# Kernel optimization log

Measured on AMD Instinct MI355X. Metric: run time of the kernel, lower is better.

## Reference

```python
import jax, jax.numpy as jnp
import numpy as np

N = 100_000   # nodes
E = 1_600_000 # edges
F = 128       # num_node_features
H = 128       # hidden_channels
C = 10        # num_classes
G = 128       # graphs in batch


def setup_inputs() -> dict:
    key = jax.random.key(0)
    ks = jax.random.split(key, 12)
    x = jax.random.normal(ks[0], (N, F), jnp.float32)
    edge_index = jax.random.randint(ks[1], (2, E), 0, N, dtype=jnp.int32)
    batch = jnp.sort(jax.random.randint(ks[2], (N,), 0, G, dtype=jnp.int32))
    s = 1.0 / np.sqrt(H)
    W0 = jax.random.normal(ks[3], (F, H), jnp.float32) * s
    b0 = jnp.zeros((H,), jnp.float32)
    W1 = jax.random.normal(ks[4], (H, H), jnp.float32) * s
    b1 = jnp.zeros((H,), jnp.float32)
    W2 = jax.random.normal(ks[5], (H, H), jnp.float32) * s
    b2 = jnp.zeros((H,), jnp.float32)
    Wlin = jax.random.normal(ks[6], (H, C), jnp.float32) * s
    blin = jnp.zeros((C,), jnp.float32)
    return {"x": x, "edge_index": edge_index, "batch": batch,
            "W0": W0, "b0": b0, "W1": W1, "b1": b1, "W2": W2, "b2": b2,
            "Wlin": Wlin, "blin": blin}


def gcn_conv(x, W, b, src, dst):
    """PyG GCNConv: symmetric-normalized aggregation with self-loops."""
    xw = x @ W  # [N, H]
    # degree from destination column, +1 for self-loop (gcn_norm)
    deg = jax.ops.segment_sum(jnp.ones(src.shape[0], xw.dtype), dst,
                              num_segments=N) + 1.0
    dinv = jax.lax.rsqrt(deg)  # deg^{-1/2}
    # edge messages: xw[src] * deg_src^{-1/2} * deg_dst^{-1/2}
    msg = xw[src] * (dinv[src] * dinv[dst])[:, None]  # [E, H]
    agg = jax.ops.segment_sum(msg, dst, num_segments=N)
    # self-loop contribution: xw * deg^{-1}
    return agg + xw * (dinv * dinv)[:, None] + b


def reference(x, edge_index, batch, W0, b0, W1, b1, W2, b2, Wlin, blin):
    src, dst = edge_index[0], edge_index[1]
    h = jax.nn.relu(gcn_conv(x, W0, b0, src, dst))
    h = jax.nn.relu(gcn_conv(h, W1, b1, src, dst))
    h = jax.nn.relu(gcn_conv(h, W2, b2, src, dst))
    # global_mean_pool over graph ids
    cnt = jax.ops.segment_sum(jnp.ones(N, h.dtype), batch, num_segments=G)
    pooled = jax.ops.segment_sum(h, batch, num_segments=G) / jnp.maximum(cnt, 1.0)[:, None]
    # dropout is identity in eval mode
    return pooled @ Wlin + blin  # [G, C]
```

## Files before the change

kernel.cpp:

```cpp
#include <hip/hip_runtime.h>

typedef short short8 __attribute__((ext_vector_type(8)));
typedef float f32x4 __attribute__((ext_vector_type(4)));

#define HDIM 128
#define SCAN_NB 256
#define SCAN_TPB 256

__device__ __forceinline__ ushort f2bf(float f) {
  uint u = __float_as_uint(f);
  u += 0x7fffu + ((u >> 16) & 1u);
  return (ushort)(u >> 16);
}
__device__ __forceinline__ float bflo(uint v){ return __uint_as_float(v << 16); }
__device__ __forceinline__ float bfhi(uint v){ return __uint_as_float(v & 0xffff0000u); }

__global__ __launch_bounds__(256) void k_deg(const int* __restrict__ dst, int E, int* __restrict__ degc) {
  for (int e = blockIdx.x*blockDim.x + threadIdx.x; e < E; e += gridDim.x*blockDim.x)
    atomicAdd(&degc[dst[e]], 1);
}

__global__ __launch_bounds__(256) void k_dinv(const int* __restrict__ degc, float* __restrict__ dinv, int N) {
  int i = blockIdx.x*256 + threadIdx.x;
  if (i < N) dinv[i] = rsqrtf((float)degc[i] + 1.0f);
}

__global__ __launch_bounds__(SCAN_TPB) void k_scanA(const int* __restrict__ degc, int N,
                                                    int* __restrict__ blocksum) {
  int ipt = (N + SCAN_NB*SCAN_TPB - 1) / (SCAN_NB*SCAN_TPB);
  int chunk = ipt * SCAN_TPB;
  int start = blockIdx.x * chunk + threadIdx.x * ipt;
  int s = 0;
  #pragma unroll
  for (int k = 0; k < 4; ++k) {
    if (k < ipt) { int i = start + k; if (i < N) s += degc[i]; }
  }
  __shared__ int red[SCAN_TPB];
  int t = threadIdx.x;
  red[t] = s; __syncthreads();
  for (int off = SCAN_TPB/2; off > 0; off >>= 1) {
    if (t < off) red[t] += red[t+off];
    __syncthreads();
  }
  if (t == 0) blocksum[blockIdx.x] = red[0];
}

__global__ __launch_bounds__(SCAN_NB) void k_scanB(const int* __restrict__ blocksum,
                                                   int* __restrict__ blockoff, int* __restrict__ totalN) {
  __shared__ int sh[SCAN_NB];
  int t = threadIdx.x;
  sh[t] = blocksum[t];
  __syncthreads();
  for (int off = 1; off < SCAN_NB; off <<= 1) {
    int v = (t >= off) ? sh[t-off] : 0;
    __syncthreads();
    sh[t] += v;
    __syncthreads();
  }
  blockoff[t] = (t == 0) ? 0 : sh[t-1];
  if (t == SCAN_NB-1) *totalN = sh[t];
}

__global__ __launch_bounds__(SCAN_TPB) void k_scanC(const int* __restrict__ degc, int N,
    const int* __restrict__ blockoff, const int* __restrict__ totalN, int* __restrict__ row_ptr) {
  int ipt = (N + SCAN_NB*SCAN_TPB - 1) / (SCAN_NB*SCAN_TPB);
  int chunk = ipt * SCAN_TPB;
  int start = blockIdx.x * chunk + threadIdx.x * ipt;
  int t = threadIdx.x;
  int vals[4];
  int s = 0;
  #pragma unroll
  for (int k = 0; k < 4; ++k) {
    int v = 0;
    if (k < ipt) { int i = start + k; if (i < N) v = degc[i]; }
    vals[k] = v; s += v;
  }
  __shared__ int sh[SCAN_TPB];
  sh[t] = s; __syncthreads();
  for (int off = 1; off < SCAN_TPB; off <<= 1) {
    int v = (t >= off) ? sh[t-off] : 0;
    __syncthreads();
    sh[t] += v;
    __syncthreads();
  }
  int run = blockoff[blockIdx.x] + ((t == 0) ? 0 : sh[t-1]);
  #pragma unroll
  for (int k = 0; k < 4; ++k) {
    if (k < ipt) { int i = start + k; if (i < N) row_ptr[i] = run; }
    run += vals[k];
  }
  if (blockIdx.x == 0 && t == 0) row_ptr[N] = *totalN;
}

__global__ __launch_bounds__(256) void k_fill(const int* __restrict__ src, const int* __restrict__ dst, int E,
    const float* __restrict__ dinv, const int* __restrict__ row_ptr, int* __restrict__ fill,
    int2* __restrict__ epack) {
  for (int e = blockIdx.x*blockDim.x + threadIdx.x; e < E; e += gridDim.x*blockDim.x) {
    int s = src[e], d = dst[e];
    int pos = row_ptr[d] + atomicAdd(&fill[d], 1);
    float cf = dinv[s] * dinv[d];
    epack[pos] = make_int2(s, __float_as_int(cf));
  }
}

template<int IN_F32>
__global__ __launch_bounds__(256,1) void k_gemm(const void* __restrict__ in_, const float* __restrict__ W,
    ushort* __restrict__ xw, int N) {
  int lane = threadIdx.x & 63;
  int wid  = (blockIdx.x * blockDim.x + threadIdx.x) >> 6;
  int nw   = (gridDim.x * blockDim.x) >> 6;
  int colB = lane & 15;
  int krow = (lane >> 4) * 8;

  short8 bfr[8][4];
  #pragma unroll
  for (int nt = 0; nt < 8; ++nt)
    #pragma unroll
    for (int kc = 0; kc < 4; ++kc) {
      short8 t;
      #pragma unroll
      for (int j = 0; j < 8; ++j)
        t[j] = (short)f2bf(W[(kc*32 + krow + j)*HDIM + nt*16 + colB]);
      bfr[nt][kc] = t;
    }

  int strips = (N + 15) >> 4;
  for (int s = wid; s < strips; s += nw) {
    int ra = s*16 + (lane & 15);
    bool va = ra < N;
    short8 a[4];
    if (IN_F32) {
      const float* xin = (const float*)in_;
      #pragma unroll
      for (int kc = 0; kc < 4; ++kc) {
        short8 t = {0,0,0,0,0,0,0,0};
        if (va) {
          const float* p = xin + (size_t)ra*HDIM + kc*32 + krow;
          float4 lo4 = *(const float4*)p;
          float4 hi4 = *(const float4*)(p+4);
          t[0]=(short)f2bf(lo4.x); t[1]=(short)f2bf(lo4.y); t[2]=(short)f2bf(lo4.z); t[3]=(short)f2bf(lo4.w);
          t[4]=(short)f2bf(hi4.x); t[5]=(short)f2bf(hi4.y); t[6]=(short)f2bf(hi4.z); t[7]=(short)f2bf(hi4.w);
        }
        a[kc] = t;
      }
    } else {
      const ushort* hin = (const ushort*)in_;
      #pragma unroll
      for (int kc = 0; kc < 4; ++kc) {
        short8 t = {0,0,0,0,0,0,0,0};
        if (va) t = *(const short8*)(hin + (size_t)ra*HDIM + kc*32 + krow);
        a[kc] = t;
      }
    }
    f32x4 acc[8];
    #pragma unroll
    for (int nt = 0; nt < 8; ++nt) { acc[nt][0]=0.f; acc[nt][1]=0.f; acc[nt][2]=0.f; acc[nt][3]=0.f; }
    #pragma unroll
    for (int nt = 0; nt < 8; ++nt)
      #pragma unroll
      for (int kc = 0; kc < 4; ++kc)
        acc[nt] = __builtin_amdgcn_mfma_f32_16x16x32_bf16(a[kc], bfr[nt][kc], acc[nt], 0, 0, 0);

    int r0 = s*16 + (lane>>4)*4;
    #pragma unroll
    for (int nt = 0; nt < 8; ++nt) {
      int c = nt*16 + (lane&15);
      #pragma unroll
      for (int rg = 0; rg < 4; ++rg) {
        int rr = r0 + rg;
        if (rr < N) xw[(size_t)rr*HDIM + c] = f2bf(acc[nt][rg]);
      }
    }
  }
}

__global__ __launch_bounds__(256) void k_agg(const uint* __restrict__ xwu, const int2* __restrict__ epack,
    const int* __restrict__ row_ptr, const float* __restrict__ dinv, const float* __restrict__ bias,
    uint* __restrict__ hu, int N) {
  int lane = threadIdx.x & 63;
  int n = blockIdx.x*4 + (threadIdx.x >> 6);
  if (n >= N) return;
  int e0 = row_ptr[n], e1 = row_ptr[n+1];
  float a0 = 0.f, a1 = 0.f;
  for (int base = e0; base < e1; base += 64) {
    int cnt = min(64, e1 - base);
    int2 myp = make_int2(0, 0);
    if (lane < cnt) myp = epack[base + lane];
    for (int j = 0; j < cnt; j += 8) {
      #pragma unroll
      for (int u = 0; u < 8; ++u) {
        int idx = j + u;
        int   sN = __shfl(myp.x, idx);
        float cf = __int_as_float(__shfl(myp.y, idx));
        uint v = xwu[(size_t)sN*64 + lane];
        a0 += cf * bflo(v);
        a1 += cf * bfhi(v);
      }
    }
  }
  float di = dinv[n]; float w = di*di;
  uint v = xwu[(size_t)n*64 + lane];
  a0 += w * bflo(v);
  a1 += w * bfhi(v);
  a0 += bias[lane*2];  a1 += bias[lane*2+1];
  a0 = fmaxf(a0, 0.f); a1 = fmaxf(a1, 0.f);
  uint o = ((uint)f2bf(a0)) | (((uint)f2bf(a1)) << 16);
  hu[(size_t)n*64 + lane] = o;
}

__global__ __launch_bounds__(256) void k_pool(const uint* __restrict__ hu, const int* __restrict__ batch,
    float* __restrict__ psum, int N) {
  int lane = threadIdx.x & 63;
  int wave = threadIdx.x >> 6;
  int n0 = blockIdx.x*512 + wave*128;
  if (n0 >= N) return;
  int n1 = min(n0 + 128, N);
  float a0 = 0.f, a1 = 0.f;
  int gc = batch[n0];
  for (int n = n0; n < n1; ++n) {
    int g = batch[n];
    if (g != gc) {
      atomicAdd(&psum[gc*HDIM + lane*2],   a0);
      atomicAdd(&psum[gc*HDIM + lane*2+1], a1);
      a0 = 0.f; a1 = 0.f; gc = g;
    }
    uint v = hu[(size_t)n*64 + lane];
    a0 += bflo(v); a1 += bfhi(v);
  }
  atomicAdd(&psum[gc*HDIM + lane*2],   a0);
  atomicAdd(&psum[gc*HDIM + lane*2+1], a1);
}

__global__ void k_bounds(const int* __restrict__ batch, int N, int G, float* __restrict__ inv_cnt) {
  __shared__ int bnd[256];
  int g = threadIdx.x;
  if (g <= G) {
    int lo = 0, hi = N;
    while (lo < hi) { int mid = (lo + hi) >> 1; if (batch[mid] < g) lo = mid + 1; else hi = mid; }
    bnd[g] = lo;
  }
  __syncthreads();
  if (g < G) {
    int c = bnd[g+1] - bnd[g];
    inv_cnt[g] = 1.0f / (float)max(c, 1);
  }
}

__global__ __launch_bounds__(256) void k_final(const float* __restrict__ psum, const float* __restrict__ inv_cnt,
    const float* __restrict__ Wlin, const float* __restrict__ blin, float* __restrict__ out, int G, int C) {
  int idx = blockIdx.x*256 + threadIdx.x;
  if (idx >= G*C) return;
  int g = idx / C, c = idx % C;
  float acc = 0.f;
  for (int k = 0; k < HDIM; ++k) acc += psum[g*HDIM + k] * Wlin[k*C + c];
  out[idx] = acc * inv_cnt[g] + blin[c];
}

extern "C" void kernel_launch(void* const* d_in, const int* in_sizes, int n_in,
                              void* d_out, int out_size, void* d_ws, size_t ws_size,
                              hipStream_t stream) {
  const float* x    = (const float*)d_in[0];
  const int*   ei   = (const int*)d_in[1];
  const int*   batch= (const int*)d_in[2];
  const float* W0   = (const float*)d_in[3];
  const float* b0   = (const float*)d_in[4];
  const float* W1   = (const float*)d_in[5];
  const float* b1   = (const float*)d_in[6];
  const float* W2   = (const float*)d_in[7];
  const float* b2   = (const float*)d_in[8];
  const float* Wlin = (const float*)d_in[9];
  const float* blin = (const float*)d_in[10];

  int N = in_sizes[0] / HDIM;
  int E = in_sizes[1] / 2;
  int C = in_sizes[10];
  int G = out_size / C;
  const int* src = ei;
  const int* dst = ei + E;

  char* ws = (char*)d_ws;
  size_t o = 0;
  auto alloc = [&](size_t bytes){ size_t r = o; o += (bytes + 511) & ~(size_t)511; return r; };
  int*    degc    = (int*)   (ws + alloc((size_t)N*4));
  float*  dinv    = (float*) (ws + alloc((size_t)N*4));
  int*    row_ptr = (int*)   (ws + alloc((size_t)(N+1)*4));
  int*    fill    = (int*)   (ws + alloc((size_t)N*4));
  float*  inv_cnt = (float*) (ws + alloc((size_t)G*4));
  int*    blocksum= (int*)   (ws + alloc((size_t)SCAN_NB*4));
  int*    blockoff= (int*)   (ws + alloc((size_t)SCAN_NB*4));
  int*    totalN  = (int*)   (ws + alloc(4));
  int2*   epack   = (int2*)  (ws + alloc((size_t)E*8));
  ushort* xw      = (ushort*)(ws + alloc((size_t)N*HDIM*2));
  ushort* hbuf    = (ushort*)(ws + alloc((size_t)N*HDIM*2));
  float*  psum    = (float*) (ws + alloc((size_t)G*HDIM*4));

  hipMemsetAsync(degc, 0, (size_t)N*4, stream);
  hipMemsetAsync(fill, 0, (size_t)N*4, stream);
  hipMemsetAsync(psum, 0, (size_t)G*HDIM*4, stream);

  k_deg  <<<2048, 256, 0, stream>>>(dst, E, degc);
  k_dinv <<<(N+255)/256, 256, 0, stream>>>(degc, dinv, N);
  k_scanA<<<SCAN_NB, SCAN_TPB, 0, stream>>>(degc, N, blocksum);
  k_scanB<<<1, SCAN_NB, 0, stream>>>(blocksum, blockoff, totalN);
  k_scanC<<<SCAN_NB, SCAN_TPB, 0, stream>>>(degc, N, blockoff, totalN, row_ptr);
  k_fill <<<2048, 256, 0, stream>>>(src, dst, E, dinv, row_ptr, fill, epack);
  k_bounds<<<1, 256, 0, stream>>>(batch, N, G, inv_cnt);

  const int gemm_blocks = 512;
  const int agg_blocks  = (N + 3) / 4;

  k_gemm<1><<<gemm_blocks, 256, 0, stream>>>((const void*)x, W0, xw, N);
  k_agg<<<agg_blocks, 256, 0, stream>>>((const uint*)xw, epack, row_ptr, dinv, b0, (uint*)hbuf, N);
  k_gemm<0><<<gemm_blocks, 256, 0, stream>>>((const void*)hbuf, W1, xw, N);
  k_agg<<<agg_blocks, 256, 0, stream>>>((const uint*)xw, epack, row_ptr, dinv, b1, (uint*)hbuf, N);
  k_gemm<0><<<gemm_blocks, 256, 0, stream>>>((const void*)hbuf, W2, xw, N);
  k_agg<<<agg_blocks, 256, 0, stream>>>((const uint*)xw, epack, row_ptr, dinv, b2, (uint*)hbuf, N);

  k_pool<<<(N + 511)/512, 256, 0, stream>>>((const uint*)hbuf, batch, psum, N);
  k_final<<<(G*C + 255)/256, 256, 0, stream>>>(psum, inv_cnt, Wlin, blin, (float*)d_out, G, C);
}
```

Before: 453.0 us.

## Co-schedule first-layer GEMM with edge CSR fill in one fused launch

The first layer's dense GEMM and the atomic CSR fill kernel are merged into one launch: one block in four runs the GEMM and the other three scatter edges. The memory-bound atomic scatter and the compute-bound MFMA GEMM can then overlap on the GPU, and one launch boundary goes away. The three workspace zeroing memsets become one by placing those buffers next to each other, and the aggregation inner loop is unrolled 16-wide instead of 8-wide. The risk is load imbalance between the two roles and __launch_bounds__(256,1) occupancy limits now also applying to the fill blocks.

```diff
diff --git a/kernel.cpp b/kernel.cpp
--- a/kernel.cpp
+++ b/kernel.cpp
@@ -92,23 +92,10 @@
   if (blockIdx.x == 0 && t == 0) row_ptr[N] = *totalN;
 }
 
-__global__ __launch_bounds__(256) void k_fill(const int* __restrict__ src, const int* __restrict__ dst, int E,
-    const float* __restrict__ dinv, const int* __restrict__ row_ptr, int* __restrict__ fill,
-    int2* __restrict__ epack) {
-  for (int e = blockIdx.x*blockDim.x + threadIdx.x; e < E; e += gridDim.x*blockDim.x) {
-    int s = src[e], d = dst[e];
-    int pos = row_ptr[d] + atomicAdd(&fill[d], 1);
-    float cf = dinv[s] * dinv[d];
-    epack[pos] = make_int2(s, __float_as_int(cf));
-  }
-}
-
 template<int IN_F32>
-__global__ __launch_bounds__(256,1) void k_gemm(const void* __restrict__ in_, const float* __restrict__ W,
-    ushort* __restrict__ xw, int N) {
+__device__ __forceinline__ void gemm_body(const void* __restrict__ in_, const float* __restrict__ W,
+    ushort* __restrict__ xw, int N, int wid, int nw) {
   int lane = threadIdx.x & 63;
-  int wid  = (blockIdx.x * blockDim.x + threadIdx.x) >> 6;
-  int nw   = (gridDim.x * blockDim.x) >> 6;
   int colB = lane & 15;
   int krow = (lane >> 4) * 8;
 
@@ -174,6 +161,37 @@
   }
 }
 
+template<int IN_F32>
+__global__ __launch_bounds__(256,1) void k_gemm(const void* __restrict__ in_, const float* __restrict__ W,
+    ushort* __restrict__ xw, int N) {
+  int wid = (blockIdx.x * blockDim.x + threadIdx.x) >> 6;
+  int nw  = (gridDim.x * blockDim.x) >> 6;
+  gemm_body<IN_F32>(in_, W, xw, N, wid, nw);
+}
+
+__global__ __launch_bounds__(256,1) void k_fuse(const float* __restrict__ x, const float* __restrict__ W0,
+    ushort* __restrict__ xw, int N,
+    const int* __restrict__ src, const int* __restrict__ dst, int E,
+    const float* __restrict__ dinv, const int* __restrict__ row_ptr, int* __restrict__ fill,
+    int2* __restrict__ epack) {
+  if ((blockIdx.x & 3) == 0) {
+    int gb  = blockIdx.x >> 2;
+    int ngb = gridDim.x >> 2;
+    int wid = (gb * 256 + threadIdx.x) >> 6;
+    int nw  = (ngb * 256) >> 6;
+    gemm_body<1>((const void*)x, W0, xw, N, wid, nw);
+  } else {
+    int fb  = blockIdx.x - ((blockIdx.x + 3) >> 2);
+    int nfb = gridDim.x - (gridDim.x >> 2);
+    for (int e = fb*256 + (int)threadIdx.x; e < E; e += nfb*256) {
+      int s = src[e], d = dst[e];
+      int pos = row_ptr[d] + atomicAdd(&fill[d], 1);
+      float cf = dinv[s] * dinv[d];
+      epack[pos] = make_int2(s, __float_as_int(cf));
+    }
+  }
+}
+
 __global__ __launch_bounds__(256) void k_agg(const uint* __restrict__ xwu, const int2* __restrict__ epack,
     const int* __restrict__ row_ptr, const float* __restrict__ dinv, const float* __restrict__ bias,
     uint* __restrict__ hu, int N) {
@@ -186,9 +204,9 @@
     int cnt = min(64, e1 - base);
     int2 myp = make_int2(0, 0);
     if (lane < cnt) myp = epack[base + lane];
-    for (int j = 0; j < cnt; j += 8) {
-      #pragma unroll
-      for (int u = 0; u < 8; ++u) {
+    for (int j = 0; j < cnt; j += 16) {
+      #pragma unroll
+      for (int u = 0; u < 16; ++u) {
         int idx = j + u;
         int   sN = __shfl(myp.x, idx);
         float cf = __int_as_float(__shfl(myp.y, idx));
@@ -281,10 +299,13 @@
   char* ws = (char*)d_ws;
   size_t o = 0;
   auto alloc = [&](size_t bytes){ size_t r = o; o += (bytes + 511) & ~(size_t)511; return r; };
+  size_t zbeg  = o;
   int*    degc    = (int*)   (ws + alloc((size_t)N*4));
+  int*    fill    = (int*)   (ws + alloc((size_t)N*4));
+  float*  psum    = (float*) (ws + alloc((size_t)G*HDIM*4));
+  size_t zend  = o;
   float*  dinv    = (float*) (ws + alloc((size_t)N*4));
   int*    row_ptr = (int*)   (ws + alloc((size_t)(N+1)*4));
-  int*    fill    = (int*)   (ws + alloc((size_t)N*4));
   float*  inv_cnt = (float*) (ws + alloc((size_t)G*4));
   int*    blocksum= (int*)   (ws + alloc((size_t)SCAN_NB*4));
   int*    blockoff= (int*)   (ws + alloc((size_t)SCAN_NB*4));
@@ -292,24 +313,21 @@
   int2*   epack   = (int2*)  (ws + alloc((size_t)E*8));
   ushort* xw      = (ushort*)(ws + alloc((size_t)N*HDIM*2));
   ushort* hbuf    = (ushort*)(ws + alloc((size_t)N*HDIM*2));
-  float*  psum    = (float*) (ws + alloc((size_t)G*HDIM*4));
-
-  hipMemsetAsync(degc, 0, (size_t)N*4, stream);
-  hipMemsetAsync(fill, 0, (size_t)N*4, stream);
-  hipMemsetAsync(psum, 0, (size_t)G*HDIM*4, stream);
+
+  hipMemsetAsync(ws + zbeg, 0, zend - zbeg, stream);
 
   k_deg  <<<2048, 256, 0, stream>>>(dst, E, degc);
   k_dinv <<<(N+255)/256, 256, 0, stream>>>(degc, dinv, N);
   k_scanA<<<SCAN_NB, SCAN_TPB, 0, stream>>>(degc, N, blocksum);
   k_scanB<<<1, SCAN_NB, 0, stream>>>(blocksum, blockoff, totalN);
   k_scanC<<<SCAN_NB, SCAN_TPB, 0, stream>>>(degc, N, blockoff, totalN, row_ptr);
-  k_fill <<<2048, 256, 0, stream>>>(src, dst, E, dinv, row_ptr, fill, epack);
   k_bounds<<<1, 256, 0, stream>>>(batch, N, G, inv_cnt);
+
+  k_fuse<<<2048, 256, 0, stream>>>(x, W0, xw, N, src, dst, E, dinv, row_ptr, fill, epack);
 
   const int gemm_blocks = 512;
   const int agg_blocks  = (N + 3) / 4;
 
-  k_gemm<1><<<gemm_blocks, 256, 0, stream>>>((const void*)x, W0, xw, N);
   k_agg<<<agg_blocks, 256, 0, stream>>>((const uint*)xw, epack, row_ptr, dinv, b0, (uint*)hbuf, N);
   k_gemm<0><<<gemm_blocks, 256, 0, stream>>>((const void*)hbuf, W1, xw, N);
   k_agg<<<agg_blocks, 256, 0, stream>>>((const uint*)xw, epack, row_ptr, dinv, b1, (uint*)hbuf, N);
```

Measured after the change: 438.7 us. 3.1% less time.

## Split wavefront into four edge groups with 16-byte row gathers in aggregation

Applied to the files above, without the earlier changes.

The aggregation kernel now splits each 64-lane wave into four 16-lane subgroups. Each subgroup handles a different edge and loads a full 256-byte bf16 row as 16-byte vectors, so every thread keeps 8 accumulators, and the partial sums are combined with cross-lane xor shuffles at the end. This aims to raise memory-level parallelism and cut the number of load instructions in the gather-bound aggregation. Separately, the three zeroed workspace buffers are placed next to each other so a single memset can clear them, removing two API calls. It costs more registers and a shuffle reduction per node, and subgroups sit idle when a node's degree is not a multiple of four.

```diff
diff --git a/kernel.cpp b/kernel.cpp
--- a/kernel.cpp
+++ b/kernel.cpp
@@ -180,32 +180,59 @@
   int lane = threadIdx.x & 63;
   int n = blockIdx.x*4 + (threadIdx.x >> 6);
   if (n >= N) return;
+  int sub = lane >> 4;
+  int li  = lane & 15;
   int e0 = row_ptr[n], e1 = row_ptr[n+1];
-  float a0 = 0.f, a1 = 0.f;
+  float acc[8];
+  #pragma unroll
+  for (int k = 0; k < 8; ++k) acc[k] = 0.f;
+
   for (int base = e0; base < e1; base += 64) {
     int cnt = min(64, e1 - base);
     int2 myp = make_int2(0, 0);
     if (lane < cnt) myp = epack[base + lane];
-    for (int j = 0; j < cnt; j += 8) {
-      #pragma unroll
-      for (int u = 0; u < 8; ++u) {
-        int idx = j + u;
-        int   sN = __shfl(myp.x, idx);
-        float cf = __int_as_float(__shfl(myp.y, idx));
-        uint v = xwu[(size_t)sN*64 + lane];
-        a0 += cf * bflo(v);
-        a1 += cf * bfhi(v);
-      }
-    }
-  }
-  float di = dinv[n]; float w = di*di;
-  uint v = xwu[(size_t)n*64 + lane];
-  a0 += w * bflo(v);
-  a1 += w * bfhi(v);
-  a0 += bias[lane*2];  a1 += bias[lane*2+1];
-  a0 = fmaxf(a0, 0.f); a1 = fmaxf(a1, 0.f);
-  uint o = ((uint)f2bf(a0)) | (((uint)f2bf(a1)) << 16);
-  hu[(size_t)n*64 + lane] = o;
+    int ng = (cnt + 3) >> 2;
+    for (int g4 = 0; g4 < ng; g4 += 4) {
+      int sN[4]; float cf[4];
+      #pragma unroll
+      for (int u = 0; u < 4; ++u) {
+        int idx = (g4 + u)*4 + sub;
+        sN[u] = __shfl(myp.x, idx);
+        cf[u] = __int_as_float(__shfl(myp.y, idx));
+      }
+      #pragma unroll
+      for (int u = 0; u < 4; ++u) {
+        const uint4 v = *(const uint4*)(xwu + (size_t)sN[u]*64 + li*4);
+        acc[0] += cf[u]*bflo(v.x); acc[1] += cf[u]*bfhi(v.x);
+        acc[2] += cf[u]*bflo(v.y); acc[3] += cf[u]*bfhi(v.y);
+        acc[4] += cf[u]*bflo(v.z); acc[5] += cf[u]*bfhi(v.z);
+        acc[6] += cf[u]*bflo(v.w); acc[7] += cf[u]*bfhi(v.w);
+      }
+    }
+  }
+  #pragma unroll
+  for (int k = 0; k < 8; ++k) {
+    acc[k] += __shfl_xor(acc[k], 16);
+    acc[k] += __shfl_xor(acc[k], 32);
+  }
+  float dn = dinv[n]; float w = dn*dn;
+  const uint4 sv = *(const uint4*)(xwu + (size_t)n*64 + li*4);
+  acc[0] += w*bflo(sv.x); acc[1] += w*bfhi(sv.x);
+  acc[2] += w*bflo(sv.y); acc[3] += w*bfhi(sv.y);
+  acc[4] += w*bflo(sv.z); acc[5] += w*bfhi(sv.z);
+  acc[6] += w*bflo(sv.w); acc[7] += w*bfhi(sv.w);
+  const float4 b4a = *(const float4*)(bias + li*8);
+  const float4 b4b = *(const float4*)(bias + li*8 + 4);
+  acc[0] += b4a.x; acc[1] += b4a.y; acc[2] += b4a.z; acc[3] += b4a.w;
+  acc[4] += b4b.x; acc[5] += b4b.y; acc[6] += b4b.z; acc[7] += b4b.w;
+  #pragma unroll
+  for (int k = 0; k < 8; ++k) acc[k] = fmaxf(acc[k], 0.f);
+  uint4 o;
+  o.x = ((uint)f2bf(acc[0])) | (((uint)f2bf(acc[1])) << 16);
+  o.y = ((uint)f2bf(acc[2])) | (((uint)f2bf(acc[3])) << 16);
+  o.z = ((uint)f2bf(acc[4])) | (((uint)f2bf(acc[5])) << 16);
+  o.w = ((uint)f2bf(acc[6])) | (((uint)f2bf(acc[7])) << 16);
+  if (sub == 0) *(uint4*)(hu + (size_t)n*64 + li*4) = o;
 }
 
 __global__ __launch_bounds__(256) void k_pool(const uint* __restrict__ hu, const int* __restrict__ batch,
@@ -281,10 +308,13 @@
   char* ws = (char*)d_ws;
   size_t o = 0;
   auto alloc = [&](size_t bytes){ size_t r = o; o += (bytes + 511) & ~(size_t)511; return r; };
+  size_t zbeg  = o;
   int*    degc    = (int*)   (ws + alloc((size_t)N*4));
+  int*    fill    = (int*)   (ws + alloc((size_t)N*4));
+  float*  psum    = (float*) (ws + alloc((size_t)G*HDIM*4));
+  size_t zend  = o;
   float*  dinv    = (float*) (ws + alloc((size_t)N*4));
   int*    row_ptr = (int*)   (ws + alloc((size_t)(N+1)*4));
-  int*    fill    = (int*)   (ws + alloc((size_t)N*4));
   float*  inv_cnt = (float*) (ws + alloc((size_t)G*4));
   int*    blocksum= (int*)   (ws + alloc((size_t)SCAN_NB*4));
   int*    blockoff= (int*)   (ws + alloc((size_t)SCAN_NB*4));
@@ -292,11 +322,8 @@
   int2*   epack   = (int2*)  (ws + alloc((size_t)E*8));
   ushort* xw      = (ushort*)(ws + alloc((size_t)N*HDIM*2));
   ushort* hbuf    = (ushort*)(ws + alloc((size_t)N*HDIM*2));
-  float*  psum    = (float*) (ws + alloc((size_t)G*HDIM*4));
-
-  hipMemsetAsync(degc, 0, (size_t)N*4, stream);
-  hipMemsetAsync(fill, 0, (size_t)N*4, stream);
-  hipMemsetAsync(psum, 0, (size_t)G*HDIM*4, stream);
+
+  hipMemsetAsync(ws + zbeg, 0, zend - zbeg, stream);
 
   k_deg  <<<2048, 256, 0, stream>>>(dst, E, degc);
   k_dinv <<<(N+255)/256, 256, 0, stream>>>(degc, dinv, N);
```

After: 457.3 us. Within noise of the previous version (+1.0%).
